# Kernel optimization log

Hardware: AMD Instinct MI355X
Metric: run time of the kernel (lower is better)

Reference implementation:

```python
import jax, jax.numpy as jnp
import numpy as np

EPS = 0.1
MAX_ITER = 10
N, IN_SIZE, IN_DIM = 16, 1024, 1024
HEADS, OUT_SIZE, OUT_DIM = 4, 128, 1024


def xavier(key, shape):
    fan_in, fan_out = shape[-1], int(np.prod(shape[:-1]))
    lim = float(np.sqrt(6.0 / (fan_in + fan_out)))
    return jax.random.uniform(key, shape, jnp.float32, -lim, lim)


def setup_inputs() -> dict:
    key = jax.random.key(0)
    k1, k2, k3 = jax.random.split(key, 3)
    x = jax.random.normal(k1, (N, IN_SIZE, IN_DIM), jnp.float32)
    ot_weight = xavier(k2, (HEADS, OUT_SIZE, IN_DIM))
    lin_w = xavier(k3, (OUT_DIM, HEADS * IN_DIM))
    lin_b = jnp.zeros((OUT_DIM,), jnp.float32)
    return {"x": x, "ot_weight": ot_weight, "lin_w": lin_w, "lin_b": lin_b}


def log_sinkhorn(K, max_iter):
    # K: [B, in_size, out_size] (already divided by eps)
    B, in_size, out_size = K.shape
    a = jnp.log(jnp.asarray(out_size / in_size, K.dtype))
    u = jnp.zeros((B, in_size), K.dtype)
    v = jnp.zeros((B, out_size), K.dtype)

    def body(carry, _):
        u, v = carry
        u = a - jax.nn.logsumexp(K + u[:, :, None] + v[:, None, :], axis=-1)
        v = -jax.nn.logsumexp(K + u[:, :, None] + v[:, None, :], axis=-2)
        return (u, v), None

    (u, v), _ = jax.lax.scan(body, (u, v), None, length=max_iter)
    return jnp.exp(K + u[:, :, None] + v[:, None, :])  # transport plan T


def reference(x, ot_weight, lin_w, lin_b):
    n, in_size, in_dim = x.shape
    m, out_size, _ = ot_weight.shape
    # similarity / eps : [n, m, in_size, out_size]
    K = jnp.einsum('nid,msd->nmis', x, ot_weight) / EPS
    T = log_sinkhorn(K.reshape(n * m, in_size, out_size), MAX_ITER)
    T = T.reshape(n, m, in_size, out_size)
    # weighted aggregation: [n, out_size, m, in_dim] -> [n, out_size, m*in_dim]
    feat = jnp.einsum('nmis,nid->nsmd', T, x).reshape(n, out_size, m * in_dim)
    # Linear + ReLU (Dropout is identity in eval mode)
    out = jax.nn.relu(feat @ lin_w.T + lin_b)
    return out
```

## Files before the change

### kernel.cpp

```cpp
#include <hip/hip_runtime.h>
#include <math.h>

#define EPSV 0.1f
#define MAX_ITER 10
constexpr int NB       = 16;
constexpr int IN_SIZE  = 1024;
constexpr int IN_DIM   = 1024;
constexpr int HEADS    = 4;
constexpr int OUT_SIZE = 128;
constexpr int OUT_DIM  = 1024;

typedef __attribute__((ext_vector_type(8))) _Float16 f16x8;
typedef __attribute__((ext_vector_type(4))) float f32x4;

__device__ __forceinline__ unsigned cvth2(float lo, float hi) {
    _Float16 a = (_Float16)lo, b = (_Float16)hi;
    unsigned short ua = *(unsigned short*)&a, ub = *(unsigned short*)&b;
    return (unsigned)ua | ((unsigned)ub << 16);
}
__device__ __forceinline__ unsigned short cvth1(float f) {
    _Float16 a = (_Float16)f;
    return *(unsigned short*)&a;
}
__device__ __forceinline__ unsigned short bf16rne(float f) {
    unsigned a = __float_as_uint(f);
    return (unsigned short)((a + 0x7fffu + ((a >> 16) & 1u)) >> 16);
}
__device__ __forceinline__ void glds16(const void* g, void* l) {
    __builtin_amdgcn_global_load_lds(
        (const __attribute__((address_space(1))) unsigned int*)g,
        (__attribute__((address_space(3))) unsigned int*)l, 16, 0, 0);
}

template<bool B_F32, int CMODE, int NF, bool SWAP, bool HMAP>
__global__ __launch_bounds__(256)
void mfma_gemm(const void* __restrict__ Ap, const void* __restrict__ Bp,
               const float* __restrict__ bias, void* __restrict__ Cp,
               int K, int lda, int ldb, int ldc, int div,
               long AsN, long AsM, long BsN, long BsM, long CsN, long CsM,
               float alpha)
{
    constexpr int BN   = NF * 32;
    constexpr int BSTR = B_F32 ? 40 : 32;
    const int z  = SWAP ? blockIdx.x : blockIdx.z;
    const int n0 = (SWAP ? blockIdx.z : blockIdx.x) * BN;
    long aoff, boff, coff;
    if (HMAP) {
        const int nn = z & 15, mm = z >> 4, bt = nn * 4 + mm;
        aoff = (long)bt * AsM; boff = (long)nn * BsN; coff = (long)bt * CsM;
    } else {
        aoff = (long)(z / div) * AsN + (long)(z % div) * AsM;
        boff = (long)(z / div) * BsN + (long)(z % div) * BsM;
        coff = (long)(z / div) * CsN + (long)(z % div) * CsM;
    }

    __shared__ short As[2][128 * 32];
    __shared__ short Bs[2][BN * BSTR];

    const int t = threadIdx.x;
    const int lane = t & 63;
    const int w = t >> 6, wr = w >> 1, wc = w & 1;
    const int lrow = lane >> 2, lce = (lane & 3) * 8;

    auto stage = [&](int buf, int k0) {
        const long abase = aoff + k0;
        const long bbase = boff + k0;
        #pragma unroll
        for (int j = 0; j < 2; ++j) {
            const int row0 = (w * 2 + j) * 16;
            glds16((const short*)Ap + abase + (long)(row0 + lrow) * lda + lce,
                   &As[buf][row0 * 32]);
        }
        if (B_F32) {
            #pragma unroll
            for (int itr = 0; itr < BN / 64; ++itr) {
                const int idx = itr * 256 + t;
                const int row = idx >> 2, kq = idx & 3;
                const float* s = (const float*)Bp + bbase + (long)(n0 + row) * ldb + kq * 8;
                const float4 f0 = *(const float4*)s, f1 = *(const float4*)(s + 4);
                uint4 p;
                p.x = cvth2(f0.x, f0.y); p.y = cvth2(f0.z, f0.w);
                p.z = cvth2(f1.x, f1.y); p.w = cvth2(f1.z, f1.w);
                *(uint4*)&Bs[buf][row * BSTR + kq * 8] = p;
            }
        } else {
            #pragma unroll
            for (int j = 0; j < BN / 64; ++j) {
                const int row0 = (w * (BN / 64) + j) * 16;
                glds16((const short*)Bp + bbase + (long)(n0 + row0 + lrow) * ldb + lce,
                       &Bs[buf][row0 * 32]);
            }
        }
    };

    f32x4 acc[4][NF];
    #pragma unroll
    for (int i = 0; i < 4; ++i)
        #pragma unroll
        for (int j = 0; j < NF; ++j) { acc[i][j].x = 0.f; acc[i][j].y = 0.f; acc[i][j].z = 0.f; acc[i][j].w = 0.f; }

    stage(0, 0);
    __syncthreads();
    int cur = 0;

    for (int k0 = 0; k0 < K; k0 += 32) {
        if (k0 + 32 < K) stage(cur ^ 1, k0 + 32);

        f16x8 af[4], bfr[NF];
        #pragma unroll
        for (int mi = 0; mi < 4; ++mi)
            af[mi] = *(const f16x8*)&As[cur][(wr * 64 + mi * 16 + (lane & 15)) * 32 + (lane >> 4) * 8];
        #pragma unroll
        for (int ni = 0; ni < NF; ++ni)
            bfr[ni] = *(const f16x8*)&Bs[cur][(wc * (BN / 2) + ni * 16 + (lane & 15)) * BSTR + (lane >> 4) * 8];
        #pragma unroll
        for (int mi = 0; mi < 4; ++mi)
            #pragma unroll
            for (int ni = 0; ni < NF; ++ni)
                acc[mi][ni] = __builtin_amdgcn_mfma_f32_16x16x32_f16(af[mi], bfr[ni], acc[mi][ni], 0, 0, 0);
        __syncthreads();
        cur ^= 1;
    }

    #pragma unroll
    for (int mi = 0; mi < 4; ++mi) {
        #pragma unroll
        for (int ni = 0; ni < NF; ++ni) {
            #pragma unroll
            for (int j = 0; j < 4; ++j) {
                const int row = wr * 64 + mi * 16 + (lane >> 4) * 4 + j;
                const int col = n0 + wc * (BN / 2) + ni * 16 + (lane & 15);
                float v = acc[mi][ni][j] * alpha;
                if (CMODE == 2) { v += bias[col]; v = fmaxf(v, 0.f); }
                if (CMODE == 2) ((float*)Cp)[coff + (long)row * ldc + col] = v;
                else ((unsigned short*)Cp)[coff + (long)row * ldc + col] = cvth1(v);
            }
        }
    }
}

__global__ __launch_bounds__(256)
void splitk_reduce(const unsigned short* __restrict__ part,
                   const float* __restrict__ bias, float* __restrict__ out)
{
    const long idx = ((long)blockIdx.x * 256 + threadIdx.x) * 8;
    const int o = (int)(idx & 1023);
    const f16x8 p0 = *(const f16x8*)(part + idx);
    const f16x8 p1 = *(const f16x8*)(part + 2097152 + idx);
    const f16x8 p2 = *(const f16x8*)(part + 2 * 2097152 + idx);
    const f16x8 p3 = *(const f16x8*)(part + 3 * 2097152 + idx);
    const float4 b0 = *(const float4*)(bias + o);
    const float4 b1 = *(const float4*)(bias + o + 4);
    float r[8];
    #pragma unroll
    for (int j = 0; j < 8; ++j) {
        const float bv = j < 4 ? (&b0.x)[j] : (&b1.x)[j - 4];
        r[j] = fmaxf((float)p0[j] + (float)p1[j] + (float)p2[j] + (float)p3[j] + bv, 0.f);
    }
    *(float4*)(out + idx)     = *(float4*)&r[0];
    *(float4*)(out + idx + 4) = *(float4*)&r[4];
}

__global__ __launch_bounds__(256)
void cvt_f16(const float* __restrict__ in, unsigned short* __restrict__ out)
{
    const long i8 = ((long)blockIdx.x * 256 + threadIdx.x) * 8;
    const float4 f0 = *(const float4*)(in + i8), f1 = *(const float4*)(in + i8 + 4);
    uint4 p;
    p.x = cvth2(f0.x, f0.y); p.y = cvth2(f0.z, f0.w);
    p.z = cvth2(f1.x, f1.y); p.w = cvth2(f1.z, f1.w);
    *(uint4*)(out + i8) = p;
}

__global__ __launch_bounds__(256)
void gemm1_exp(const unsigned short* __restrict__ otwH, const float* __restrict__ x,
               unsigned short* __restrict__ ekb, float* __restrict__ MiB,
               unsigned short* __restrict__ xTo)
{
    const int zb = blockIdx.x;
    const int nn = zb & 15, mm = zb >> 4;
    const int bt = nn * 4 + mm;
    const unsigned short* A = otwH + (long)mm * (OUT_SIZE * IN_DIM);
    const float* B = x + (long)nn * (IN_SIZE * IN_DIM);
    const int n0 = blockIdx.z * 128;

    __shared__ short As[2][128 * 32];
    __shared__ short Bs[2][128 * 40];
    __shared__ float colmax[2][128];

    const int t = threadIdx.x;
    const int lane = t & 63;
    const int w = t >> 6, wr = w >> 1, wc = w & 1;
    const int lrow = lane >> 2, lce = (lane & 3) * 8;

    auto stage = [&](int buf, int k0) {
        #pragma unroll
        for (int j = 0; j < 2; ++j) {
            const int row0 = (w * 2 + j) * 16;
            glds16(A + (long)(row0 + lrow) * 1024 + k0 + lce, &As[buf][row0 * 32]);
        }
        #pragma unroll
        for (int itr = 0; itr < 2; ++itr) {
            const int idx = itr * 256 + t;
            const int row = idx >> 2, kq = idx & 3;
            const float* s = B + (long)(n0 + row) * 1024 + k0 + kq * 8;
            const float4 f0 = *(const float4*)s, f1 = *(const float4*)(s + 4);
            uint4 p;
            p.x = cvth2(f0.x, f0.y); p.y = cvth2(f0.z, f0.w);
            p.z = cvth2(f1.x, f1.y); p.w = cvth2(f1.z, f1.w);
            *(uint4*)&Bs[buf][row * 40 + kq * 8] = p;
        }
    };

    f32x4 acc[4][4];
    #pragma unroll
    for (int i = 0; i < 4; ++i)
        #pragma unroll
        for (int j = 0; j < 4; ++j) { acc[i][j].x = 0.f; acc[i][j].y = 0.f; acc[i][j].z = 0.f; acc[i][j].w = 0.f; }

    stage(0, 0);
    __syncthreads();
    int cur = 0;

    unsigned short* xTn = xTo + (long)nn * (IN_SIZE * IN_DIM);

    for (int k0 = 0; k0 < 1024; k0 += 32) {
        if (k0 + 32 < 1024) stage(cur ^ 1, k0 + 32);

        f16x8 af[4], bfr[4];
        #pragma unroll
        for (int mi = 0; mi < 4; ++mi)
            af[mi] = *(const f16x8*)&As[cur][(wr * 64 + mi * 16 + (lane & 15)) * 32 + (lane >> 4) * 8];
        #pragma unroll
        for (int ni = 0; ni < 4; ++ni)
            bfr[ni] = *(const f16x8*)&Bs[cur][(wc * 64 + ni * 16 + (lane & 15)) * 40 + (lane >> 4) * 8];
        #pragma unroll
        for (int mi = 0; mi < 4; ++mi)
            #pragma unroll
            for (int ni = 0; ni < 4; ++ni)
                acc[mi][ni] = __builtin_amdgcn_mfma_f32_16x16x32_f16(af[mi], bfr[ni], acc[mi][ni], 0, 0, 0);

        if ((k0 >> 8) == mm) {
            const int dl = t & 31;
            const int ig = (t >> 5) * 16;
            unsigned short tmp[16];
            #pragma unroll
            for (int j = 0; j < 16; ++j)
                tmp[j] = (unsigned short)Bs[cur][(ig + j) * 40 + dl];
            unsigned short* dst = xTn + (long)(k0 + dl) * IN_SIZE + n0 + ig;
            *(uint4*)dst       = *(uint4*)&tmp[0];
            *(uint4*)(dst + 8) = *(uint4*)&tmp[8];
        }
        __syncthreads();
        cur ^= 1;
    }

    float lm[4];
    #pragma unroll
    for (int ni = 0; ni < 4; ++ni) {
        float mx = -INFINITY;
        #pragma unroll
        for (int mi = 0; mi < 4; ++mi)
            #pragma unroll
            for (int j = 0; j < 4; ++j) mx = fmaxf(mx, acc[mi][ni][j]);
        mx *= 10.0f;
        mx = fmaxf(mx, __shfl_xor(mx, 16, 64));
        mx = fmaxf(mx, __shfl_xor(mx, 32, 64));
        lm[ni] = mx;
    }
    if ((lane >> 4) == 0) {
        #pragma unroll
        for (int ni = 0; ni < 4; ++ni) colmax[wr][wc * 64 + ni * 16 + lane] = lm[ni];
    }
    __syncthreads();
    float cm[4];
    #pragma unroll
    for (int ni = 0; ni < 4; ++ni) {
        const int c = wc * 64 + ni * 16 + (lane & 15);
        cm[ni] = fmaxf(colmax[0][c], colmax[1][c]);
    }
    if (wr == 0 && (lane >> 4) == 0) {
        #pragma unroll
        for (int ni = 0; ni < 4; ++ni)
            MiB[(long)bt * 1024 + n0 + wc * 64 + ni * 16 + lane] = cm[ni];
    }
    unsigned short* ekz = ekb + (long)bt * (OUT_SIZE * IN_SIZE);
    #pragma unroll
    for (int mi = 0; mi < 4; ++mi) {
        #pragma unroll
        for (int ni = 0; ni < 4; ++ni) {
            const int col = n0 + wc * 64 + ni * 16 + (lane & 15);
            #pragma unroll
            for (int j = 0; j < 4; ++j) {
                const int row = wr * 64 + mi * 16 + (lane >> 4) * 4 + j;
                ekz[(long)row * 1024 + col] = bf16rne(__expf(fmaf(acc[mi][ni][j], 10.f, -cm[ni])));
            }
        }
    }
}

__global__ __launch_bounds__(1024)
void sinkhorn_split(unsigned short* __restrict__ ekb,
                    const float* __restrict__ MiB,
                    float* __restrict__ xchg, unsigned int* __restrict__ ctr)
{
    const int b = blockIdx.x;
    const int q = blockIdx.z;
    const int t = threadIdx.x;
    const int lane = t & 63, w = t >> 6;

    __shared__ unsigned ekw[128 * 129];
    __shared__ float part_u[8][256];
    __shared__ float part_v[8][128];
    __shared__ float eu_l[256];
    __shared__ float v_s[128], ev_s[128];
    __shared__ float red8[8];
    __shared__ float wg_s;

    {
        const unsigned short* src = ekb + (long)b * 131072 + q * 256;
        #pragma unroll
        for (int j = 0; j < 4; ++j) {
            const int idx = t + 1024 * j;
            const int s = idx >> 5, c8 = (idx & 31) * 8;
            const uint4 p = *(const uint4*)(src + (long)s * 1024 + c8);
            const int bd = s * 129 + (c8 >> 1);
            ekw[bd] = p.x; ekw[bd + 1] = p.y; ekw[bd + 2] = p.z; ekw[bd + 3] = p.w;
        }
    }
    float mi_t = 0.f, u_reg = 0.f, w_t = 0.f;
    if (t < 256) mi_t = MiB[(long)b * 1024 + q * 256 + t];
    if (t < 128) { v_s[t] = 0.f; ev_s[t] = 1.0f; }
    __syncthreads();

    const float A0 = -2.0794415416798357f;
    float vmx = 0.f;

    for (int it = 0; it < MAX_ITER; ++it) {
        {
            const int p = t & 127, sq = t >> 7;
            float s0 = 0.f, s1 = 0.f;
            #pragma unroll
            for (int j = 0; j < 16; ++j) {
                const int s = sq * 16 + j;
                const unsigned e = ekw[s * 129 + p];
                const float evv = ev_s[s];
                s0 = fmaf(__uint_as_float(e << 16),          evv, s0);
                s1 = fmaf(__uint_as_float(e & 0xffff0000u),  evv, s1);
            }
            part_u[sq][2 * p]     = s0;
            part_u[sq][2 * p + 1] = s1;
        }
        __syncthreads();

        if (t < 256) {
            float S = part_u[0][t];
            #pragma unroll
            for (int g = 1; g < 8; ++g) S += part_u[g][t];
            const float un = A0 - u_reg - mi_t - vmx - __logf(S);
            u_reg = un;
            w_t = mi_t + un;
            float wl = w_t;
            #pragma unroll
            for (int m = 1; m < 64; m <<= 1) wl = fmaxf(wl, __shfl_xor(wl, m, 64));
            if (lane == 0) red8[4 + w] = wl;
        }
        __syncthreads();
        const float wmx_l = fmaxf(fmaxf(red8[4], red8[5]), fmaxf(red8[6], red8[7]));
        if (t < 256) eu_l[t] = __expf(w_t - wmx_l);
        __syncthreads();

        {
            const int s = t & 127, g = t >> 7;
            float acc = 0.f;
            #pragma unroll
            for (int j = 0; j < 16; ++j) {
                const int p = 16 * g + j;
                const unsigned e = ekw[s * 129 + p];
                const float2 eup = *(const float2*)&eu_l[2 * p];
                acc = fmaf(__uint_as_float(e << 16),         eup.x, acc);
                acc = fmaf(__uint_as_float(e & 0xffff0000u), eup.y, acc);
            }
            part_v[g][s] = acc;
        }
        __syncthreads();

        float* slot = xchg + ((long)(b * MAX_ITER + it) * 4 + q) * 160;
        if (t < 128) {
            float cp_l = part_v[0][t];
            #pragma unroll
            for (int g = 1; g < 8; ++g) cp_l += part_v[g][t];
            __hip_atomic_store(slot + t, cp_l, __ATOMIC_RELAXED, __HIP_MEMORY_SCOPE_AGENT);
        }
        if (t == 0)
            __hip_atomic_store(slot + 128, wmx_l, __ATOMIC_RELAXED, __HIP_MEMORY_SCOPE_AGENT);
        __syncthreads();
        if (t == 0) {
            unsigned int* c = ctr + b * MAX_ITER + it;
            __hip_atomic_fetch_add(c, 1u, __ATOMIC_RELEASE, __HIP_MEMORY_SCOPE_AGENT);
            while (__hip_atomic_load(c, __ATOMIC_RELAXED, __HIP_MEMORY_SCOPE_AGENT) < 4u) {}
            (void)__hip_atomic_load(c, __ATOMIC_ACQUIRE, __HIP_MEMORY_SCOPE_AGENT);
        }
        __syncthreads();

        if (t < 128) {
            float* base = xchg + (long)(b * MAX_ITER + it) * 4 * 160;
            const float w0 = __hip_atomic_load(base + 0 * 160 + 128, __ATOMIC_RELAXED, __HIP_MEMORY_SCOPE_AGENT);
            const float w1 = __hip_atomic_load(base + 1 * 160 + 128, __ATOMIC_RELAXED, __HIP_MEMORY_SCOPE_AGENT);
            const float w2 = __hip_atomic_load(base + 2 * 160 + 128, __ATOMIC_RELAXED, __HIP_MEMORY_SCOPE_AGENT);
            const float w3 = __hip_atomic_load(base + 3 * 160 + 128, __ATOMIC_RELAXED, __HIP_MEMORY_SCOPE_AGENT);
            const float wg = fmaxf(fmaxf(w0, w1), fmaxf(w2, w3));
            const float c0 = __hip_atomic_load(base + 0 * 160 + t, __ATOMIC_RELAXED, __HIP_MEMORY_SCOPE_AGENT);
            const float c1 = __hip_atomic_load(base + 1 * 160 + t, __ATOMIC_RELAXED, __HIP_MEMORY_SCOPE_AGENT);
            const float c2 = __hip_atomic_load(base + 2 * 160 + t, __ATOMIC_RELAXED, __HIP_MEMORY_SCOPE_AGENT);
            const float c3 = __hip_atomic_load(base + 3 * 160 + t, __ATOMIC_RELAXED, __HIP_MEMORY_SCOPE_AGENT);
            const float cp = c0 * __expf(w0 - wg) + c1 * __expf(w1 - wg)
                           + c2 * __expf(w2 - wg) + c3 * __expf(w3 - wg);
            const float vn = -v_s[t] - wg - __logf(cp);
            v_s[t] = vn;
            if (t == 0) wg_s = wg;
            float xv = vn;
            #pragma unroll
            for (int m = 1; m < 64; m <<= 1) xv = fmaxf(xv, __shfl_xor(xv, m, 64));
            if (lane == 0) red8[w] = xv;
        }
        __syncthreads();
        vmx = fmaxf(red8[0], red8[1]);
        if (t < 128) ev_s[t] = __expf(v_s[t] - vmx);
        __syncthreads();
    }

    const float wg = wg_s;
    if (t < 256) eu_l[t] = __expf(w_t - wg);
    if (t < 128) ev_s[t] = __expf(v_s[t] + wg);
    __syncthreads();
    unsigned short* To = ekb + (long)b * 131072 + q * 256;
    #pragma unroll
    for (int j = 0; j < 16; ++j) {
        const int idx = t + 1024 * j;
        const int s  = idx >> 7;
        const int ip = idx & 127;
        const unsigned e = ekw[s * 129 + ip];
        const float2 eup = *(const float2*)&eu_l[2 * ip];
        const float ec = ev_s[s];
        const float lo = __uint_as_float(e << 16)         * eup.x * ec;
        const float hi = __uint_as_float(e & 0xffff0000u) * eup.y * ec;
        *(unsigned*)(To + (long)s * 1024 + ip * 2) = cvth2(lo, hi);
    }
}

extern "C" void kernel_launch(void* const* d_in, const int* in_sizes, int n_in,
                              void* d_out, int out_size, void* d_ws, size_t ws_size,
                              hipStream_t stream)
{
    const float* x     = (const float*)d_in[0];
    const float* otw   = (const float*)d_in[1];
    const float* lin_w = (const float*)d_in[2];
    const float* lin_b = (const float*)d_in[3];
    float* out = (float*)d_out;

    unsigned short* xT   = (unsigned short*)d_ws;
    unsigned short* ekb  = xT + 16777216;
    unsigned short* feat = ekb + 8388608;
    unsigned short* partial = (unsigned short*)d_ws;
    float* MiB  = (float*)d_out;
    float* xchg = MiB + 131072;
    unsigned int* ctrB = (unsigned int*)(MiB + 655360);
    unsigned short* otwH = (unsigned short*)(MiB + 786432);

    hipMemsetAsync(ctrB, 0, 64 * MAX_ITER * sizeof(unsigned int), stream);

    cvt_f16<<<dim3(256), 256, 0, stream>>>(otw, otwH);

    gemm1_exp<<<dim3(64, 1, 8), 256, 0, stream>>>(otwH, x, ekb, MiB, xT);

    sinkhorn_split<<<dim3(64, 1, 4), 1024, 0, stream>>>(ekb, MiB, xchg, ctrB);

    mfma_gemm<false, 1, 2, true, true><<<dim3(64, 1, 16), 256, 0, stream>>>(
        ekb, xT, nullptr, feat,
        1024, 1024, 1024, 1024, 4,
        0, 131072, 1048576, 0, 0, 131072, 1.0f);

    mfma_gemm<true, 1, 2, false, false><<<dim3(16, 1, 64), 256, 0, stream>>>(
        feat, lin_w, nullptr, partial,
        1024, 1024, 4096, 1024, 16,
        131072, 524288, 1024, 0, 2097152, 131072, 1.0f);

    splitk_reduce<<<dim3(1024), 256, 0, stream>>>(partial, lin_b, out);
}
```

Baseline: 175.3 us.

## Fuse similarity GEMM with Sinkhorn iterations in one kernel

Merges the first GEMM+exp kernel and the split Sinkhorn kernel into a single 512-thread kernel. Each block now computes a 128x256 tile of the similarity matrix and writes the exponentiated bf16 values straight into shared memory, then runs the Sinkhorn iterations in place. This removes the global round trip of the exp(K) matrix and the per-column max array, plus one launch. In exchange the GEMM grid drops from 512 to 256 blocks, shared memory per block grows, and the Sinkhorn phase runs with half as many threads per block.

```diff
diff --git a/kernel.cpp b/kernel.cpp
--- a/kernel.cpp
+++ b/kernel.cpp
@@ -172,36 +172,48 @@
     *(uint4*)(out + i8) = p;
 }
 
-__global__ __launch_bounds__(256)
-void gemm1_exp(const unsigned short* __restrict__ otwH, const float* __restrict__ x,
-               unsigned short* __restrict__ ekb, float* __restrict__ MiB,
-               unsigned short* __restrict__ xTo)
+__global__ __launch_bounds__(512)
+void gemm1_sinkhorn(const unsigned short* __restrict__ otwH,
+                    const float* __restrict__ x,
+                    unsigned short* __restrict__ Tb,
+                    unsigned short* __restrict__ xTo,
+                    float* __restrict__ xchg, unsigned int* __restrict__ ctr)
 {
-    const int zb = blockIdx.x;
-    const int nn = zb & 15, mm = zb >> 4;
+    const int hm = blockIdx.x;
+    const int nn = hm & 15, mm = hm >> 4;
     const int bt = nn * 4 + mm;
+    const int q  = blockIdx.z;
+    const int n0 = q * 256;
+
     const unsigned short* A = otwH + (long)mm * (OUT_SIZE * IN_DIM);
     const float* B = x + (long)nn * (IN_SIZE * IN_DIM);
-    const int n0 = blockIdx.z * 128;
 
     __shared__ short As[2][128 * 32];
-    __shared__ short Bs[2][128 * 40];
-    __shared__ float colmax[2][128];
+    __shared__ short Bs[2][256 * 40];
+    __shared__ unsigned ekw[128 * 129];
+    __shared__ float part_u[4][256];
+    __shared__ float part_v[4][128];
+    __shared__ float eu_l[256];
+    __shared__ float Mi_s[256];
+    __shared__ float v_s[128], ev_s[128];
+    __shared__ float colmax[2][256];
+    __shared__ float red8[8];
+    __shared__ float wg_s;
 
     const int t = threadIdx.x;
     const int lane = t & 63;
-    const int w = t >> 6, wr = w >> 1, wc = w & 1;
+    const int w = t >> 6;
+    const int wr = w >> 2, wc = w & 3;
     const int lrow = lane >> 2, lce = (lane & 3) * 8;
 
     auto stage = [&](int buf, int k0) {
-        #pragma unroll
-        for (int j = 0; j < 2; ++j) {
-            const int row0 = (w * 2 + j) * 16;
+        {
+            const int row0 = w * 16;
             glds16(A + (long)(row0 + lrow) * 1024 + k0 + lce, &As[buf][row0 * 32]);
         }
         #pragma unroll
         for (int itr = 0; itr < 2; ++itr) {
-            const int idx = itr * 256 + t;
+            const int idx = itr * 512 + t;
             const int row = idx >> 2, kq = idx & 3;
             const float* s = B + (long)(n0 + row) * 1024 + k0 + kq * 8;
             const float4 f0 = *(const float4*)s, f1 = *(const float4*)(s + 4);
@@ -255,82 +267,49 @@
         cur ^= 1;
     }
 
-    float lm[4];
-    #pragma unroll
-    for (int ni = 0; ni < 4; ++ni) {
-        float mx = -INFINITY;
-        #pragma unroll
-        for (int mi = 0; mi < 4; ++mi)
-            #pragma unroll
-            for (int j = 0; j < 4; ++j) mx = fmaxf(mx, acc[mi][ni][j]);
-        mx *= 10.0f;
-        mx = fmaxf(mx, __shfl_xor(mx, 16, 64));
-        mx = fmaxf(mx, __shfl_xor(mx, 32, 64));
-        lm[ni] = mx;
-    }
-    if ((lane >> 4) == 0) {
-        #pragma unroll
-        for (int ni = 0; ni < 4; ++ni) colmax[wr][wc * 64 + ni * 16 + lane] = lm[ni];
-    }
-    __syncthreads();
-    float cm[4];
-    #pragma unroll
-    for (int ni = 0; ni < 4; ++ni) {
-        const int c = wc * 64 + ni * 16 + (lane & 15);
-        cm[ni] = fmaxf(colmax[0][c], colmax[1][c]);
-    }
-    if (wr == 0 && (lane >> 4) == 0) {
-        #pragma unroll
-        for (int ni = 0; ni < 4; ++ni)
-            MiB[(long)bt * 1024 + n0 + wc * 64 + ni * 16 + lane] = cm[ni];
-    }
-    unsigned short* ekz = ekb + (long)bt * (OUT_SIZE * IN_SIZE);
-    #pragma unroll
-    for (int mi = 0; mi < 4; ++mi) {
+    {
+        float lm[4];
         #pragma unroll
         for (int ni = 0; ni < 4; ++ni) {
-            const int col = n0 + wc * 64 + ni * 16 + (lane & 15);
-            #pragma unroll
-            for (int j = 0; j < 4; ++j) {
-                const int row = wr * 64 + mi * 16 + (lane >> 4) * 4 + j;
-                ekz[(long)row * 1024 + col] = bf16rne(__expf(fmaf(acc[mi][ni][j], 10.f, -cm[ni])));
-            }
-        }
-    }
-}
-
-__global__ __launch_bounds__(1024)
-void sinkhorn_split(unsigned short* __restrict__ ekb,
-                    const float* __restrict__ MiB,
-                    float* __restrict__ xchg, unsigned int* __restrict__ ctr)
-{
-    const int b = blockIdx.x;
-    const int q = blockIdx.z;
-    const int t = threadIdx.x;
-    const int lane = t & 63, w = t >> 6;
-
-    __shared__ unsigned ekw[128 * 129];
-    __shared__ float part_u[8][256];
-    __shared__ float part_v[8][128];
-    __shared__ float eu_l[256];
-    __shared__ float v_s[128], ev_s[128];
-    __shared__ float red8[8];
-    __shared__ float wg_s;
+            float mx = -INFINITY;
+            #pragma unroll
+            for (int mi = 0; mi < 4; ++mi)
+                #pragma unroll
+                for (int j = 0; j < 4; ++j) mx = fmaxf(mx, acc[mi][ni][j]);
+            mx *= 10.0f;
+            mx = fmaxf(mx, __shfl_xor(mx, 16, 64));
+            mx = fmaxf(mx, __shfl_xor(mx, 32, 64));
+            lm[ni] = mx;
+        }
+        if ((lane >> 4) == 0) {
+            #pragma unroll
+            for (int ni = 0; ni < 4; ++ni)
+                colmax[wr][wc * 64 + ni * 16 + lane] = lm[ni];
+        }
+    }
+    __syncthreads();
+    if (t < 256) Mi_s[t] = fmaxf(colmax[0][t], colmax[1][t]);
+    if (t < 128) { v_s[t] = 0.f; ev_s[t] = 1.0f; }
+    __syncthreads();
 
     {
-        const unsigned short* src = ekb + (long)b * 131072 + q * 256;
-        #pragma unroll
-        for (int j = 0; j < 4; ++j) {
-            const int idx = t + 1024 * j;
-            const int s = idx >> 5, c8 = (idx & 31) * 8;
-            const uint4 p = *(const uint4*)(src + (long)s * 1024 + c8);
-            const int bd = s * 129 + (c8 >> 1);
-            ekw[bd] = p.x; ekw[bd + 1] = p.y; ekw[bd + 2] = p.z; ekw[bd + 3] = p.w;
-        }
-    }
-    float mi_t = 0.f, u_reg = 0.f, w_t = 0.f;
-    if (t < 256) mi_t = MiB[(long)b * 1024 + q * 256 + t];
-    if (t < 128) { v_s[t] = 0.f; ev_s[t] = 1.0f; }
+        unsigned short* ek16 = (unsigned short*)ekw;
+        #pragma unroll
+        for (int ni = 0; ni < 4; ++ni) {
+            const int col = wc * 64 + ni * 16 + (lane & 15);
+            const float mi_c = Mi_s[col];
+            #pragma unroll
+            for (int mi = 0; mi < 4; ++mi) {
+                #pragma unroll
+                for (int j = 0; j < 4; ++j) {
+                    const int row = wr * 64 + mi * 16 + (lane >> 4) * 4 + j;
+                    ek16[row * 258 + col] = bf16rne(__expf(fmaf(acc[mi][ni][j], 10.f, -mi_c)));
+                }
+            }
+        }
+    }
+    float u_reg = 0.f, w_t = 0.f;
+    const float mi_t = (t < 256) ? Mi_s[t] : 0.f;
     __syncthreads();
 
     const float A0 = -2.0794415416798357f;
@@ -341,8 +320,8 @@
             const int p = t & 127, sq = t >> 7;
             float s0 = 0.f, s1 = 0.f;
             #pragma unroll
-            for (int j = 0; j < 16; ++j) {
-                const int s = sq * 16 + j;
+            for (int j = 0; j < 32; ++j) {
+                const int s = sq * 32 + j;
                 const unsigned e = ekw[s * 129 + p];
                 const float evv = ev_s[s];
                 s0 = fmaf(__uint_as_float(e << 16),          evv, s0);
@@ -354,9 +333,7 @@
         __syncthreads();
 
         if (t < 256) {
-            float S = part_u[0][t];
-            #pragma unroll
-            for (int g = 1; g < 8; ++g) S += part_u[g][t];
+            const float S = part_u[0][t] + part_u[1][t] + part_u[2][t] + part_u[3][t];
             const float un = A0 - u_reg - mi_t - vmx - __logf(S);
             u_reg = un;
             w_t = mi_t + un;
@@ -372,31 +349,29 @@
 
         {
             const int s = t & 127, g = t >> 7;
-            float acc = 0.f;
-            #pragma unroll
-            for (int j = 0; j < 16; ++j) {
-                const int p = 16 * g + j;
+            float acc2 = 0.f;
+            #pragma unroll
+            for (int j = 0; j < 32; ++j) {
+                const int p = 32 * g + j;
                 const unsigned e = ekw[s * 129 + p];
                 const float2 eup = *(const float2*)&eu_l[2 * p];
-                acc = fmaf(__uint_as_float(e << 16),         eup.x, acc);
-                acc = fmaf(__uint_as_float(e & 0xffff0000u), eup.y, acc);
-            }
-            part_v[g][s] = acc;
-        }
-        __syncthreads();
-
-        float* slot = xchg + ((long)(b * MAX_ITER + it) * 4 + q) * 160;
+                acc2 = fmaf(__uint_as_float(e << 16),         eup.x, acc2);
+                acc2 = fmaf(__uint_as_float(e & 0xffff0000u), eup.y, acc2);
+            }
+            part_v[g][s] = acc2;
+        }
+        __syncthreads();
+
+        float* slot = xchg + ((long)(bt * MAX_ITER + it) * 4 + q) * 160;
         if (t < 128) {
-            float cp_l = part_v[0][t];
-            #pragma unroll
-            for (int g = 1; g < 8; ++g) cp_l += part_v[g][t];
+            const float cp_l = part_v[0][t] + part_v[1][t] + part_v[2][t] + part_v[3][t];
             __hip_atomic_store(slot + t, cp_l, __ATOMIC_RELAXED, __HIP_MEMORY_SCOPE_AGENT);
         }
         if (t == 0)
             __hip_atomic_store(slot + 128, wmx_l, __ATOMIC_RELAXED, __HIP_MEMORY_SCOPE_AGENT);
         __syncthreads();
         if (t == 0) {
-            unsigned int* c = ctr + b * MAX_ITER + it;
+            unsigned int* c = ctr + bt * MAX_ITER + it;
             __hip_atomic_fetch_add(c, 1u, __ATOMIC_RELEASE, __HIP_MEMORY_SCOPE_AGENT);
             while (__hip_atomic_load(c, __ATOMIC_RELAXED, __HIP_MEMORY_SCOPE_AGENT) < 4u) {}
             (void)__hip_atomic_load(c, __ATOMIC_ACQUIRE, __HIP_MEMORY_SCOPE_AGENT);
@@ -404,7 +379,7 @@
         __syncthreads();
 
         if (t < 128) {
-            float* base = xchg + (long)(b * MAX_ITER + it) * 4 * 160;
+            float* base = xchg + (long)(bt * MAX_ITER + it) * 4 * 160;
             const float w0 = __hip_atomic_load(base + 0 * 160 + 128, __ATOMIC_RELAXED, __HIP_MEMORY_SCOPE_AGENT);
             const float w1 = __hip_atomic_load(base + 1 * 160 + 128, __ATOMIC_RELAXED, __HIP_MEMORY_SCOPE_AGENT);
             const float w2 = __hip_atomic_load(base + 2 * 160 + 128, __ATOMIC_RELAXED, __HIP_MEMORY_SCOPE_AGENT);
@@ -434,10 +409,10 @@
     if (t < 256) eu_l[t] = __expf(w_t - wg);
     if (t < 128) ev_s[t] = __expf(v_s[t] + wg);
     __syncthreads();
-    unsigned short* To = ekb + (long)b * 131072 + q * 256;
+    unsigned short* To = Tb + (long)bt * 131072 + q * 256;
     #pragma unroll
-    for (int j = 0; j < 16; ++j) {
-        const int idx = t + 1024 * j;
+    for (int j = 0; j < 32; ++j) {
+        const int idx = t + 512 * j;
         const int s  = idx >> 7;
         const int ip = idx & 127;
         const unsigned e = ekw[s * 129 + ip];
@@ -460,24 +435,23 @@
     float* out = (float*)d_out;
 
     unsigned short* xT   = (unsigned short*)d_ws;
-    unsigned short* ekb  = xT + 16777216;
-    unsigned short* feat = ekb + 8388608;
+    unsigned short* Tb   = xT + 16777216;
+    unsigned short* feat = Tb + 8388608;
     unsigned short* partial = (unsigned short*)d_ws;
-    float* MiB  = (float*)d_out;
-    float* xchg = MiB + 131072;
-    unsigned int* ctrB = (unsigned int*)(MiB + 655360);
-    unsigned short* otwH = (unsigned short*)(MiB + 786432);
+    float* base = (float*)d_out;
+    float* xchg = base + 131072;
+    unsigned int* ctrB = (unsigned int*)(base + 655360);
+    unsigned short* otwH = (unsigned short*)(base + 786432);
 
     hipMemsetAsync(ctrB, 0, 64 * MAX_ITER * sizeof(unsigned int), stream);
 
     cvt_f16<<<dim3(256), 256, 0, stream>>>(otw, otwH);
 
-    gemm1_exp<<<dim3(64, 1, 8), 256, 0, stream>>>(otwH, x, ekb, MiB, xT);
-
-    sinkhorn_split<<<dim3(64, 1, 4), 1024, 0, stream>>>(ekb, MiB, xchg, ctrB);
+    gemm1_sinkhorn<<<dim3(64, 1, 4), 512, 0, stream>>>(
+        otwH, x, Tb, xT, xchg, ctrB);
 
     mfma_gemm<false, 1, 2, true, true><<<dim3(64, 1, 16), 256, 0, stream>>>(
-        ekb, xT, nullptr, feat,
+        Tb, xT, nullptr, feat,
         1024, 1024, 1024, 1024, 4,
         0, 131072, 1048576, 0, 0, 131072, 1.0f);
 
```

Measured after the change: 178.9 us. 2.1% more time.
